# Optimization experiments

Measured on AMD Instinct MI355X. Metric: run time of the kernel, lower is better.

## Reference

```python
import jax, jax.numpy as jnp
import numpy as np

D = 32          # embedding_size
B = 16384       # batch_size
P = 16          # neighbor_sample_size (paths per item per hop)
NE = 100000     # n_entity
NU = 100000     # n_user
NR = 32         # n_relation
N_ITER = 2


def setup_inputs() -> dict:
    key = jax.random.key(0)
    ks = jax.random.split(key, 20)
    s = 0.1
    nrm = lambda k, sh: jax.random.normal(k, sh, dtype=jnp.float32) * s
    inp = {
        "user_table": nrm(ks[0], (NU, D)),
        "ent_table": nrm(ks[1], (NE, D)),
        "rel_table": nrm(ks[2], (NR, D)),
        # PyTorch LSTM params, gate order (i, f, g, o)
        "w_ih0": nrm(ks[3], (4 * D, 2 * D)),
        "w_hh0": nrm(ks[4], (4 * D, D)),
        "b_ih0": nrm(ks[5], (4 * D,)),
        "b_hh0": nrm(ks[6], (4 * D,)),
        "w_ih1": nrm(ks[7], (4 * D, 2 * D)),
        "w_hh1": nrm(ks[8], (4 * D, D)),
        "b_ih1": nrm(ks[9], (4 * D,)),
        "b_hh1": nrm(ks[10], (4 * D,)),
        "agg_w": nrm(ks[11], (D, D)),
        "agg_b": nrm(ks[12], (D,)),
        "users": jax.random.randint(ks[13], (B,), 0, NU),
        "items": jax.random.randint(ks[14], (B,), 0, NE),
        "ratings": jax.random.randint(ks[15], (B,), 0, 2),
        # hop h path table: [n_entity, P, 2*(h+1)+1]; values < 32 valid for both tables
        "lp0": jax.random.randint(ks[16], (NE, P, 3), 0, 32),
        "lp1": jax.random.randint(ks[17], (NE, P, 5), 0, 32),
    }
    return inp


def _lstm_last(seq, w_ih, w_hh, b_ih, b_hh):
    # seq: [N, T, 2D] -> final hidden state [N, D], PyTorch gate order i,f,g,o
    N = seq.shape[0]
    H = w_hh.shape[1]
    bias = b_ih + b_hh

    def step(carry, x):
        h, c = carry
        g = x @ w_ih.T + h @ w_hh.T + bias
        i, f, gg, o = jnp.split(g, 4, axis=-1)
        c = jax.nn.sigmoid(f) * c + jax.nn.sigmoid(i) * jnp.tanh(gg)
        h = jax.nn.sigmoid(o) * jnp.tanh(c)
        return (h, c), None

    h0 = jnp.zeros((N, H), seq.dtype)
    (h, _), _ = jax.lax.scan(step, (h0, h0), jnp.swapaxes(seq, 0, 1))
    return h


def _forward(user_table, ent_table, rel_table, lstm_params, agg_w, agg_b,
             users, items, ratings, lps):
    u = user_table[users]                # [B, D]
    items_emb = ent_table[items]         # [B, D]
    for hop in range(N_ITER):
        lp = lps[hop]
        w_ih, w_hh, b_ih, b_hh = lstm_params[hop]
        il = lp[items]                   # [B, P, 2*(hop+1)+1]
        seed_e = ent_table[il[:, :, 0]]  # [B, P, D]
        u_b = jnp.broadcast_to(u[:, None, :], seed_e.shape)
        first = jnp.concatenate([u_b, seed_e], -1)[:, :, None, :]   # [B,P,1,2D]
        rel_e = rel_table[il[:, :, 1::2]]                            # [B,P,hop+1,D]
        tail_e = ent_table[il[:, :, 2::2]]                           # [B,P,hop+1,D]
        rest = jnp.concatenate([rel_e, tail_e], -1)                  # [B,P,hop+1,2D]
        seq = jnp.concatenate([first, rest], 2).reshape(B * P, hop + 2, 2 * D)
        h = _lstm_last(seq, w_ih, w_hh, b_ih, b_hh)                  # [B*P, D]
        final = h.reshape(B, P, D).sum(axis=1)                       # hidden_out sum
        items_emb = (items_emb + final) @ agg_w.T + agg_b            # 'sum' aggregator
    scores = jnp.sum(u * items_emb, axis=-1)                         # [B]
    r = ratings.astype(scores.dtype)
    # stable BCE on sigmoid(scores)
    loss = -jnp.mean(r * jax.nn.log_sigmoid(scores) + (1.0 - r) * jax.nn.log_sigmoid(-scores))
    return loss, jax.nn.sigmoid(scores)


def reference(user_table, ent_table, rel_table,
              w_ih0, w_hh0, b_ih0, b_hh0,
              w_ih1, w_hh1, b_ih1, b_hh1,
              agg_w, agg_b,
              users, items, ratings, lp0, lp1):
    lstm_params = [(w_ih0, w_hh0, b_ih0, b_hh0), (w_ih1, w_hh1, b_ih1, b_hh1)]
    loss, scores_normalized = _forward(user_table, ent_table, rel_table,
                                       lstm_params, agg_w, agg_b,
                                       users, items, ratings, (lp0, lp1))
    return (loss, scores_normalized, items)
```

## Files before the change

### kernel.cpp

```cpp
#include <hip/hip_runtime.h>
#include <math.h>

#define D  32
#define BN 16384
#define PP 16

typedef __bf16 bf16x8 __attribute__((ext_vector_type(8)));
typedef float  floatx4 __attribute__((ext_vector_type(4)));

#define IMG_BYTES   29184
#define WIH_OFF     0
#define WHH_OFF     18432
#define BIAS_OFF    28672
#define X_OFF       29184
#define H_OFF       38400
#define LDS_BYTES   43520

__device__ __forceinline__ float sigf(float x) {
    float e = __builtin_amdgcn_exp2f(-x * 1.44269504088896341f);
    return __builtin_amdgcn_rcpf(1.0f + e);
}
__device__ __forceinline__ float tanh_fast(float x) {
    float e = __builtin_amdgcn_exp2f(x * 2.88539008177792681f);
    return 1.0f - 2.0f * __builtin_amdgcn_rcpf(e + 1.0f);
}
__device__ __forceinline__ float logsigf(float x) {
    float ax = fabsf(x);
    float l = log1pf(__expf(-ax));
    return (x >= 0.0f) ? -l : x - l;
}

__device__ __forceinline__ void stage16(const float* __restrict__ src, char* dst) {
    const float4* s = (const float4*)src;
    float4 a = s[0], b = s[1], c = s[2], d = s[3];
    bf16x8 lo = { (__bf16)a.x, (__bf16)a.y, (__bf16)a.z, (__bf16)a.w,
                  (__bf16)b.x, (__bf16)b.y, (__bf16)b.z, (__bf16)b.w };
    bf16x8 hi = { (__bf16)c.x, (__bf16)c.y, (__bf16)c.z, (__bf16)c.w,
                  (__bf16)d.x, (__bf16)d.y, (__bf16)d.z, (__bf16)d.w };
    *(bf16x8*)dst        = lo;
    *(bf16x8*)(dst + 16) = hi;
}

__global__ __launch_bounds__(256)
void prep_weights(const float* __restrict__ w_ih, const float* __restrict__ w_hh,
                  const float* __restrict__ b_ih, const float* __restrict__ b_hh,
                  float* __restrict__ img_f)
{
    char* base = (char*)img_f;
    const int t0 = blockIdx.x * 256 + threadIdx.x;
    for (int idx = t0; idx < 8192; idx += 2048) {
        int n = idx >> 6, k = idx & 63;
        ((__bf16*)(base + WIH_OFF))[n * 72 + k] = (__bf16)w_ih[idx];
    }
    for (int idx = t0; idx < 4096; idx += 2048) {
        int n = idx >> 5, k = idx & 31;
        ((__bf16*)(base + WHH_OFF))[n * 40 + k] = (__bf16)w_hh[idx];
    }
    if (t0 < 128)
        ((float*)(base + BIAS_OFF))[t0] = b_ih[t0] + b_hh[t0];
}

template<int L, int T>
__global__ __launch_bounds__(256, 2)
void hop_mfma(const float* __restrict__ user_table,
              const float* __restrict__ ent_table,
              const float* __restrict__ rel_table,
              const float* __restrict__ img,
              const int*   __restrict__ users,
              const int*   __restrict__ items,
              const int*   __restrict__ lp,
              float* __restrict__ final_out)
{
    __shared__ __align__(16) char lds[LDS_BYTES];

    const int tid  = threadIdx.x;
    const int lane = tid & 63;
    const int wave = tid >> 6;

    {
        const float4* g = (const float4*)img;
        float4* l = (float4*)lds;
        #pragma unroll
        for (int i = 0; i < 8; ++i) {
            int idx = i * 256 + tid;
            if (idx < IMG_BYTES / 16) l[idx] = g[idx];
        }
    }
    __syncthreads();

    char* Wih  = lds + WIH_OFF;
    char* Whh  = lds + WHH_OFF;
    const float* bias = (const float*)(lds + BIAS_OFF);
    char* Xl   = lds + X_OFF;
    char* Hl   = lds + H_OFF;

    const int srow  = tid >> 2;
    const int squad = tid & 3;
    const int spair = blockIdx.x * 64 + srow;
    const int sb    = spair >> 4;
    const int sp    = spair & 15;
    const int sitem = items[sb];
    const int suser = users[sb];
    const int* __restrict__ sil = lp + ((size_t)sitem * PP + sp) * L;
    char* sdst = Xl + srow * 144 + squad * 32;

    const int wrow = wave * 16;
    const int am   = wrow + (lane & 15);
    const int ak   = (lane >> 4) * 8;
    const int bnl  = lane & 15;

    float cst[8]  = {0,0,0,0,0,0,0,0};
    float hout[8];
    floatx4 acc[8];
    #pragma unroll
    for (int nt = 0; nt < 8; ++nt) {
        float bv = bias[nt * 16 + bnl];
        floatx4 v = { bv, bv, bv, bv };
        acc[nt] = v;
    }

    #pragma unroll
    for (int t = 0; t < T; ++t) {
        {
            const float* src;
            if (t == 0) {
                src = (squad < 2) ? user_table + (size_t)suser * D + squad * 16
                                  : ent_table + (size_t)sil[0] * D + (squad - 2) * 16;
            } else {
                src = (squad < 2) ? rel_table + (size_t)sil[2 * t - 1] * D + squad * 16
                                  : ent_table + (size_t)sil[2 * t]     * D + (squad - 2) * 16;
            }
            stage16(src, sdst);
        }

        bf16x8 ax0 = *(const bf16x8*)(Xl + am * 144 + ak * 2);
        bf16x8 ax1 = *(const bf16x8*)(Xl + am * 144 + 64 + ak * 2);
        bf16x8 ah  = {};
        if (t > 0) ah = *(const bf16x8*)(Hl + am * 80 + ak * 2);

        #pragma unroll
        for (int nt = 0; nt < 8; ++nt) {
            const int bn = nt * 16 + bnl;
            bf16x8 b0 = *(const bf16x8*)(Wih + bn * 144 + ak * 2);
            bf16x8 b1 = *(const bf16x8*)(Wih + bn * 144 + 64 + ak * 2);
            floatx4 a = acc[nt];
            a = __builtin_amdgcn_mfma_f32_16x16x32_bf16(ax0, b0, a, 0, 0, 0);
            a = __builtin_amdgcn_mfma_f32_16x16x32_bf16(ax1, b1, a, 0, 0, 0);
            if (t > 0) {
                bf16x8 bh = *(const bf16x8*)(Whh + bn * 80 + ak * 2);
                a = __builtin_amdgcn_mfma_f32_16x16x32_bf16(ah, bh, a, 0, 0, 0);
            }
            acc[nt] = a;
        }

        #pragma unroll
        for (int ng = 0; ng < 2; ++ng) {
            floatx4 gi = acc[ng], gf = acc[ng + 2], gg = acc[ng + 4], go = acc[ng + 6];
            #pragma unroll
            for (int r = 0; r < 4; ++r) {
                float c = cst[ng * 4 + r];
                c = sigf(gf[r]) * c + sigf(gi[r]) * tanh_fast(gg[r]);
                cst[ng * 4 + r] = c;
                float h = sigf(go[r]) * tanh_fast(c);
                hout[ng * 4 + r] = h;
                if (t < T - 1) {
                    int pr = wrow + (lane >> 4) * 4 + r;
                    int un = ng * 16 + bnl;
                    *(__bf16*)(Hl + pr * 80 + un * 2) = (__bf16)h;
                }
            }
        }

        if (t < T - 1) {
            #pragma unroll
            for (int nt = 0; nt < 8; ++nt) {
                float bv = bias[nt * 16 + bnl];
                floatx4 v = { bv, bv, bv, bv };
                acc[nt] = v;
            }
        }
    }

    const int fb = blockIdx.x * 4 + wave;
    #pragma unroll
    for (int ng = 0; ng < 2; ++ng) {
        float v = hout[ng * 4 + 0] + hout[ng * 4 + 1] + hout[ng * 4 + 2] + hout[ng * 4 + 3];
        v += __shfl_xor(v, 16);
        v += __shfl_xor(v, 32);
        if (lane < 16)
            final_out[(size_t)fb * D + ng * 16 + lane] = v;
    }
}

__global__ __launch_bounds__(256)
void agg_kernel(const float* __restrict__ src_emb,
                const float* __restrict__ ent_table,
                const int*   __restrict__ items,
                const float* __restrict__ final_in,
                const float* __restrict__ agg_w,
                const float* __restrict__ agg_b,
                float* __restrict__ out_emb)
{
    const int t = blockIdx.x * 256 + threadIdx.x;
    const int b = t >> 5;
    const int j = t & 31;
    const float* __restrict__ src =
        src_emb ? (src_emb + (size_t)b * D) : (ent_table + (size_t)items[b] * D);
    const float* __restrict__ fin = final_in + (size_t)b * D;
    const float* __restrict__ w   = agg_w + (size_t)j * D;
    float acc = agg_b[j];
    #pragma unroll
    for (int k = 0; k < D; ++k) acc = fmaf(src[k] + fin[k], w[k], acc);
    out_emb[t] = acc;
}

__global__ __launch_bounds__(256)
void score_kernel(const float* __restrict__ user_table,
                  const float* __restrict__ emb,
                  const int*   __restrict__ users,
                  const int*   __restrict__ items,
                  const int*   __restrict__ ratings,
                  float* __restrict__ out,
                  float* __restrict__ partials)
{
    __shared__ float red[4];
    const int t = threadIdx.x;
    const int b = blockIdx.x * 256 + t;
    const float* __restrict__ u = user_table + (size_t)users[b] * D;
    const float* __restrict__ e = emb + (size_t)b * D;
    float s = 0.0f;
    #pragma unroll
    for (int k = 0; k < D; ++k) s = fmaf(u[k], e[k], s);
    out[1 + b]      = sigf(s);
    out[1 + BN + b] = (float)items[b];
    float r = (float)ratings[b];
    float term = r * logsigf(s) + (1.0f - r) * logsigf(-s);
    #pragma unroll
    for (int m = 1; m < 64; m <<= 1) term += __shfl_xor(term, m);
    if ((t & 63) == 0) red[t >> 6] = term;
    __syncthreads();
    if (t == 0) partials[blockIdx.x] = red[0] + red[1] + red[2] + red[3];
}

__global__ void loss_kernel(const float* __restrict__ partials, float* __restrict__ out)
{
    const int t = threadIdx.x;
    float v = partials[t];
    #pragma unroll
    for (int m = 1; m < 64; m <<= 1) v += __shfl_xor(v, m);
    if (t == 0) out[0] = -v / (float)BN;
}

extern "C" void kernel_launch(void* const* d_in, const int* in_sizes, int n_in,
                              void* d_out, int out_size, void* d_ws, size_t ws_size,
                              hipStream_t stream)
{
    const float* user_table = (const float*)d_in[0];
    const float* ent_table  = (const float*)d_in[1];
    const float* rel_table  = (const float*)d_in[2];
    const float* w_ih0 = (const float*)d_in[3];
    const float* w_hh0 = (const float*)d_in[4];
    const float* b_ih0 = (const float*)d_in[5];
    const float* b_hh0 = (const float*)d_in[6];
    const float* w_ih1 = (const float*)d_in[7];
    const float* w_hh1 = (const float*)d_in[8];
    const float* b_ih1 = (const float*)d_in[9];
    const float* b_hh1 = (const float*)d_in[10];
    const float* agg_w = (const float*)d_in[11];
    const float* agg_b = (const float*)d_in[12];
    const int* users   = (const int*)d_in[13];
    const int* items   = (const int*)d_in[14];
    const int* ratings = (const int*)d_in[15];
    const int* lp0     = (const int*)d_in[16];
    const int* lp1     = (const int*)d_in[17];
    float* out = (float*)d_out;

    float* ws        = (float*)d_ws;
    float* final_buf = ws;
    float* emb0      = ws + (size_t)BN * D;
    float* emb1      = ws + 2 * (size_t)BN * D;
    float* partials  = ws + 3 * (size_t)BN * D;
    float* img0      = ws + 3 * (size_t)BN * D + 64;
    float* img1      = img0 + IMG_BYTES / 4;

    prep_weights<<<8, 256, 0, stream>>>(w_ih0, w_hh0, b_ih0, b_hh0, img0);
    prep_weights<<<8, 256, 0, stream>>>(w_ih1, w_hh1, b_ih1, b_hh1, img1);

    const int hop_blocks = (BN * PP) / 64;
    hop_mfma<3, 2><<<hop_blocks, 256, 0, stream>>>(
        user_table, ent_table, rel_table, img0, users, items, lp0, final_buf);
    agg_kernel<<<(BN * D) / 256, 256, 0, stream>>>(
        nullptr, ent_table, items, final_buf, agg_w, agg_b, emb0);
    hop_mfma<5, 3><<<hop_blocks, 256, 0, stream>>>(
        user_table, ent_table, rel_table, img1, users, items, lp1, final_buf);
    agg_kernel<<<(BN * D) / 256, 256, 0, stream>>>(
        emb0, ent_table, items, final_buf, agg_w, agg_b, emb1);
    score_kernel<<<BN / 256, 256, 0, stream>>>(
        user_table, emb1, users, items, ratings, out, partials);
    loss_kernel<<<1, 64, 0, stream>>>(partials, out);
}
```

Measured before the change: 249.3 us.

## Fuse both LSTM hops into one launch and fuse aggregation with scoring

Runs both hop LSTMs in a single kernel, with interleaved blocks selecting the hop, since the hop-1 LSTM does not depend on hop-0 results. Input fragments are loaded directly from global memory into MFMA registers instead of being staged through LDS. Gate activations are rewritten to share reciprocals. Both aggregation steps and scoring are fused into one kernel, and the weight prep launches are merged. This cuts launch count and intermediate global traffic, at the cost of some uncoalesced gathers and mixed workloads within one grid.

```diff
diff --git a/kernel.cpp b/kernel.cpp
--- a/kernel.cpp
+++ b/kernel.cpp
@@ -8,21 +8,19 @@
 typedef __bf16 bf16x8 __attribute__((ext_vector_type(8)));
 typedef float  floatx4 __attribute__((ext_vector_type(4)));
 
-#define IMG_BYTES   29184
 #define WIH_OFF     0
 #define WHH_OFF     18432
 #define BIAS_OFF    28672
-#define X_OFF       29184
-#define H_OFF       38400
-#define LDS_BYTES   43520
+#define IMG_BYTES   29184
+#define H_OFF       IMG_BYTES
+#define LDS_BYTES   (IMG_BYTES + 5120)
+
+#define K1 1.44269504088896341f
+#define K2 2.88539008177792681f
 
 __device__ __forceinline__ float sigf(float x) {
-    float e = __builtin_amdgcn_exp2f(-x * 1.44269504088896341f);
+    float e = __builtin_amdgcn_exp2f(-x * K1);
     return __builtin_amdgcn_rcpf(1.0f + e);
-}
-__device__ __forceinline__ float tanh_fast(float x) {
-    float e = __builtin_amdgcn_exp2f(x * 2.88539008177792681f);
-    return 1.0f - 2.0f * __builtin_amdgcn_rcpf(e + 1.0f);
 }
 __device__ __forceinline__ float logsigf(float x) {
     float ax = fabsf(x);
@@ -30,24 +28,31 @@
     return (x >= 0.0f) ? -l : x - l;
 }
 
-__device__ __forceinline__ void stage16(const float* __restrict__ src, char* dst) {
-    const float4* s = (const float4*)src;
-    float4 a = s[0], b = s[1], c = s[2], d = s[3];
-    bf16x8 lo = { (__bf16)a.x, (__bf16)a.y, (__bf16)a.z, (__bf16)a.w,
-                  (__bf16)b.x, (__bf16)b.y, (__bf16)b.z, (__bf16)b.w };
-    bf16x8 hi = { (__bf16)c.x, (__bf16)c.y, (__bf16)c.z, (__bf16)c.w,
-                  (__bf16)d.x, (__bf16)d.y, (__bf16)d.z, (__bf16)d.w };
-    *(bf16x8*)dst        = lo;
-    *(bf16x8*)(dst + 16) = hi;
+__device__ __forceinline__ bf16x8 cvt8(float4 lo, float4 hi) {
+    bf16x8 r = { (__bf16)lo.x, (__bf16)lo.y, (__bf16)lo.z, (__bf16)lo.w,
+                 (__bf16)hi.x, (__bf16)hi.y, (__bf16)hi.z, (__bf16)hi.w };
+    return r;
+}
+__device__ __forceinline__ bf16x8 load_frag(const float* __restrict__ tab,
+                                            int row, int ak) {
+    const float4* p = (const float4*)(tab + (size_t)row * D) + (ak >> 2);
+    return cvt8(p[0], p[1]);
 }
 
 __global__ __launch_bounds__(256)
-void prep_weights(const float* __restrict__ w_ih, const float* __restrict__ w_hh,
-                  const float* __restrict__ b_ih, const float* __restrict__ b_hh,
-                  float* __restrict__ img_f)
-{
-    char* base = (char*)img_f;
-    const int t0 = blockIdx.x * 256 + threadIdx.x;
+void prep_weights(const float* __restrict__ w_ih0, const float* __restrict__ w_hh0,
+                  const float* __restrict__ b_ih0, const float* __restrict__ b_hh0,
+                  const float* __restrict__ w_ih1, const float* __restrict__ w_hh1,
+                  const float* __restrict__ b_ih1, const float* __restrict__ b_hh1,
+                  float* __restrict__ img0, float* __restrict__ img1)
+{
+    const bool second = blockIdx.x >= 8;
+    const float* w_ih = second ? w_ih1 : w_ih0;
+    const float* w_hh = second ? w_hh1 : w_hh0;
+    const float* b_ih = second ? b_ih1 : b_ih0;
+    const float* b_hh = second ? b_hh1 : b_hh0;
+    char* base = (char*)(second ? img1 : img0);
+    const int t0 = (blockIdx.x & 7) * 256 + threadIdx.x;
     for (int idx = t0; idx < 8192; idx += 2048) {
         int n = idx >> 6, k = idx & 63;
         ((__bf16*)(base + WIH_OFF))[n * 72 + k] = (__bf16)w_ih[idx];
@@ -60,195 +65,217 @@
         ((float*)(base + BIAS_OFF))[t0] = b_ih[t0] + b_hh[t0];
 }
 
-template<int L, int T>
+template<bool FIRST, bool LAST>
+__device__ __forceinline__ void lstm_step(
+    const char* __restrict__ Wih, const char* __restrict__ Whh, char* __restrict__ Hl,
+    bf16x8 ax0, bf16x8 ax1, const float* __restrict__ biasv,
+    float* __restrict__ cst, float* __restrict__ hout,
+    int bnl, int ak, int am, int wrow, int lane)
+{
+    bf16x8 ah = {};
+    if (!FIRST) ah = *(const bf16x8*)(Hl + am * 80 + ak * 2);
+
+    floatx4 acc[8];
+    #pragma unroll
+    for (int nt = 0; nt < 8; ++nt) {
+        floatx4 v = { biasv[nt], biasv[nt], biasv[nt], biasv[nt] };
+        acc[nt] = v;
+    }
+    #pragma unroll
+    for (int nt = 0; nt < 8; ++nt) {
+        const int bn = nt * 16 + bnl;
+        bf16x8 b0 = *(const bf16x8*)(Wih + bn * 144 + ak * 2);
+        bf16x8 b1 = *(const bf16x8*)(Wih + bn * 144 + 64 + ak * 2);
+        floatx4 a = acc[nt];
+        a = __builtin_amdgcn_mfma_f32_16x16x32_bf16(ax0, b0, a, 0, 0, 0);
+        a = __builtin_amdgcn_mfma_f32_16x16x32_bf16(ax1, b1, a, 0, 0, 0);
+        if (!FIRST) {
+            bf16x8 bh = *(const bf16x8*)(Whh + bn * 80 + ak * 2);
+            a = __builtin_amdgcn_mfma_f32_16x16x32_bf16(ah, bh, a, 0, 0, 0);
+        }
+        acc[nt] = a;
+    }
+
+    #pragma unroll
+    for (int ng = 0; ng < 2; ++ng) {
+        floatx4 gi = acc[ng], gf = acc[ng + 2], gg = acc[ng + 4], go = acc[ng + 6];
+        #pragma unroll
+        for (int r = 0; r < 4; ++r) {
+            float Ai = 1.0f + __builtin_amdgcn_exp2f(-gi[r] * K1);
+            float Af = 1.0f + __builtin_amdgcn_exp2f(-gf[r] * K1);
+            float G2 = __builtin_amdgcn_exp2f(gg[r] * K2);
+            float Gp = G2 + 1.0f, Gm = G2 - 1.0f;
+            float cold = FIRST ? 0.0f : cst[ng * 4 + r];
+            float num = cold * Ai * Gp + Gm * Af;
+            float c = num * __builtin_amdgcn_rcpf(Af * Ai * Gp);
+            cst[ng * 4 + r] = c;
+            float Ao = 1.0f + __builtin_amdgcn_exp2f(-go[r] * K1);
+            float C2 = __builtin_amdgcn_exp2f(c * K2);
+            float h = (C2 - 1.0f) * __builtin_amdgcn_rcpf(Ao * (C2 + 1.0f));
+            hout[ng * 4 + r] = h;
+            if (!LAST) {
+                int pr = wrow + (lane >> 4) * 4 + r;
+                *(__bf16*)(Hl + pr * 80 + (ng * 16 + bnl) * 2) = (__bf16)h;
+            }
+        }
+    }
+}
+
 __global__ __launch_bounds__(256, 2)
 void hop_mfma(const float* __restrict__ user_table,
               const float* __restrict__ ent_table,
               const float* __restrict__ rel_table,
-              const float* __restrict__ img,
+              const float* __restrict__ img0,
+              const float* __restrict__ img1,
               const int*   __restrict__ users,
               const int*   __restrict__ items,
-              const int*   __restrict__ lp,
-              float* __restrict__ final_out)
+              const int*   __restrict__ lp0,
+              const int*   __restrict__ lp1,
+              float* __restrict__ F0,
+              float* __restrict__ F1)
 {
     __shared__ __align__(16) char lds[LDS_BYTES];
 
+    const bool second = blockIdx.x & 1;
+    const int  idx    = blockIdx.x >> 1;
     const int tid  = threadIdx.x;
     const int lane = tid & 63;
     const int wave = tid >> 6;
 
     {
-        const float4* g = (const float4*)img;
+        const float4* g = (const float4*)(second ? img1 : img0);
         float4* l = (float4*)lds;
         #pragma unroll
         for (int i = 0; i < 8; ++i) {
-            int idx = i * 256 + tid;
-            if (idx < IMG_BYTES / 16) l[idx] = g[idx];
+            int k = i * 256 + tid;
+            if (k < IMG_BYTES / 16) l[k] = g[k];
         }
     }
-    __syncthreads();
-
-    char* Wih  = lds + WIH_OFF;
-    char* Whh  = lds + WHH_OFF;
-    const float* bias = (const float*)(lds + BIAS_OFF);
-    char* Xl   = lds + X_OFF;
-    char* Hl   = lds + H_OFF;
-
-    const int srow  = tid >> 2;
-    const int squad = tid & 3;
-    const int spair = blockIdx.x * 64 + srow;
-    const int sb    = spair >> 4;
-    const int sp    = spair & 15;
-    const int sitem = items[sb];
-    const int suser = users[sb];
-    const int* __restrict__ sil = lp + ((size_t)sitem * PP + sp) * L;
-    char* sdst = Xl + srow * 144 + squad * 32;
-
+
+    const char* Wih = lds + WIH_OFF;
+    const char* Whh = lds + WHH_OFF;
+    char* Hl = lds + H_OFF;
+
+    const int bnl  = lane & 15;
+    const int ak   = (lane >> 4) * 8;
     const int wrow = wave * 16;
-    const int am   = wrow + (lane & 15);
-    const int ak   = (lane >> 4) * 8;
-    const int bnl  = lane & 15;
-
-    float cst[8]  = {0,0,0,0,0,0,0,0};
-    float hout[8];
-    floatx4 acc[8];
-    #pragma unroll
-    for (int nt = 0; nt < 8; ++nt) {
-        float bv = bias[nt * 16 + bnl];
-        floatx4 v = { bv, bv, bv, bv };
-        acc[nt] = v;
-    }
-
-    #pragma unroll
-    for (int t = 0; t < T; ++t) {
-        {
-            const float* src;
-            if (t == 0) {
-                src = (squad < 2) ? user_table + (size_t)suser * D + squad * 16
-                                  : ent_table + (size_t)sil[0] * D + (squad - 2) * 16;
-            } else {
-                src = (squad < 2) ? rel_table + (size_t)sil[2 * t - 1] * D + squad * 16
-                                  : ent_table + (size_t)sil[2 * t]     * D + (squad - 2) * 16;
-            }
-            stage16(src, sdst);
+    const int am   = wrow + bnl;
+
+    const int fb   = idx * 4 + wave;
+    const int item = items[fb];
+    const int user = users[fb];
+    const int* __restrict__ il = (second ? lp1 : lp0)
+        + ((size_t)item * PP + bnl) * (second ? 5 : 3);
+
+    bf16x8 xa0, xb0, xa1, xb1, xa2 = {}, xb2 = {};
+    {
+        const int i0 = il[0];
+        xa0 = load_frag(user_table, user, ak);
+        xb0 = load_frag(ent_table, i0, ak);
+        const int i1 = il[1], i2 = il[2];
+        xa1 = load_frag(rel_table, i1, ak);
+        xb1 = load_frag(ent_table, i2, ak);
+        if (second) {
+            const int i3 = il[3], i4 = il[4];
+            xa2 = load_frag(rel_table, i3, ak);
+            xb2 = load_frag(ent_table, i4, ak);
         }
-
-        bf16x8 ax0 = *(const bf16x8*)(Xl + am * 144 + ak * 2);
-        bf16x8 ax1 = *(const bf16x8*)(Xl + am * 144 + 64 + ak * 2);
-        bf16x8 ah  = {};
-        if (t > 0) ah = *(const bf16x8*)(Hl + am * 80 + ak * 2);
-
+    }
+
+    __syncthreads();
+
+    float biasv[8];
+    {
+        const float* bias = (const float*)(lds + BIAS_OFF);
         #pragma unroll
-        for (int nt = 0; nt < 8; ++nt) {
-            const int bn = nt * 16 + bnl;
-            bf16x8 b0 = *(const bf16x8*)(Wih + bn * 144 + ak * 2);
-            bf16x8 b1 = *(const bf16x8*)(Wih + bn * 144 + 64 + ak * 2);
-            floatx4 a = acc[nt];
-            a = __builtin_amdgcn_mfma_f32_16x16x32_bf16(ax0, b0, a, 0, 0, 0);
-            a = __builtin_amdgcn_mfma_f32_16x16x32_bf16(ax1, b1, a, 0, 0, 0);
-            if (t > 0) {
-                bf16x8 bh = *(const bf16x8*)(Whh + bn * 80 + ak * 2);
-                a = __builtin_amdgcn_mfma_f32_16x16x32_bf16(ah, bh, a, 0, 0, 0);
-            }
-            acc[nt] = a;
-        }
-
-        #pragma unroll
-        for (int ng = 0; ng < 2; ++ng) {
-            floatx4 gi = acc[ng], gf = acc[ng + 2], gg = acc[ng + 4], go = acc[ng + 6];
-            #pragma unroll
-            for (int r = 0; r < 4; ++r) {
-                float c = cst[ng * 4 + r];
-                c = sigf(gf[r]) * c + sigf(gi[r]) * tanh_fast(gg[r]);
-                cst[ng * 4 + r] = c;
-                float h = sigf(go[r]) * tanh_fast(c);
-                hout[ng * 4 + r] = h;
-                if (t < T - 1) {
-                    int pr = wrow + (lane >> 4) * 4 + r;
-                    int un = ng * 16 + bnl;
-                    *(__bf16*)(Hl + pr * 80 + un * 2) = (__bf16)h;
-                }
-            }
-        }
-
-        if (t < T - 1) {
-            #pragma unroll
-            for (int nt = 0; nt < 8; ++nt) {
-                float bv = bias[nt * 16 + bnl];
-                floatx4 v = { bv, bv, bv, bv };
-                acc[nt] = v;
-            }
-        }
-    }
-
-    const int fb = blockIdx.x * 4 + wave;
+        for (int nt = 0; nt < 8; ++nt) biasv[nt] = bias[nt * 16 + bnl];
+    }
+
+    float cst[8], hout[8];
+    lstm_step<true, false>(Wih, Whh, Hl, xa0, xb0, biasv, cst, hout, bnl, ak, am, wrow, lane);
+    if (!second) {
+        lstm_step<false, true>(Wih, Whh, Hl, xa1, xb1, biasv, cst, hout, bnl, ak, am, wrow, lane);
+    } else {
+        lstm_step<false, false>(Wih, Whh, Hl, xa1, xb1, biasv, cst, hout, bnl, ak, am, wrow, lane);
+        lstm_step<false, true >(Wih, Whh, Hl, xa2, xb2, biasv, cst, hout, bnl, ak, am, wrow, lane);
+    }
+
+    float* Fout = second ? F1 : F0;
     #pragma unroll
     for (int ng = 0; ng < 2; ++ng) {
         float v = hout[ng * 4 + 0] + hout[ng * 4 + 1] + hout[ng * 4 + 2] + hout[ng * 4 + 3];
         v += __shfl_xor(v, 16);
         v += __shfl_xor(v, 32);
         if (lane < 16)
-            final_out[(size_t)fb * D + ng * 16 + lane] = v;
+            Fout[(size_t)fb * D + ng * 16 + lane] = v;
     }
 }
 
 __global__ __launch_bounds__(256)
-void agg_kernel(const float* __restrict__ src_emb,
-                const float* __restrict__ ent_table,
-                const int*   __restrict__ items,
-                const float* __restrict__ final_in,
-                const float* __restrict__ agg_w,
-                const float* __restrict__ agg_b,
-                float* __restrict__ out_emb)
-{
-    const int t = blockIdx.x * 256 + threadIdx.x;
-    const int b = t >> 5;
-    const int j = t & 31;
-    const float* __restrict__ src =
-        src_emb ? (src_emb + (size_t)b * D) : (ent_table + (size_t)items[b] * D);
-    const float* __restrict__ fin = final_in + (size_t)b * D;
-    const float* __restrict__ w   = agg_w + (size_t)j * D;
-    float acc = agg_b[j];
-    #pragma unroll
-    for (int k = 0; k < D; ++k) acc = fmaf(src[k] + fin[k], w[k], acc);
-    out_emb[t] = acc;
+void chain_score(const float* __restrict__ user_table,
+                 const float* __restrict__ ent_table,
+                 const float* __restrict__ agg_w,
+                 const float* __restrict__ agg_b,
+                 const int*   __restrict__ users,
+                 const int*   __restrict__ items,
+                 const int*   __restrict__ ratings,
+                 const float* __restrict__ F0,
+                 const float* __restrict__ F1,
+                 float* __restrict__ out,
+                 float* __restrict__ partials)
+{
+    __shared__ float s[8][33];
+    __shared__ float red[8];
+    const int tid = threadIdx.x;
+    const int bb  = tid >> 5;
+    const int j   = tid & 31;
+    const int b   = blockIdx.x * 8 + bb;
+    const int it  = items[b];
+
+    s[bb][j] = ent_table[(size_t)it * D + j] + F0[(size_t)b * D + j];
+    __syncthreads();
+    const float* __restrict__ w = agg_w + (size_t)j * D;
+    float e0 = agg_b[j];
+    #pragma unroll
+    for (int k = 0; k < D; ++k) e0 = fmaf(s[bb][k], w[k], e0);
+    __syncthreads();
+    s[bb][j] = e0 + F1[(size_t)b * D + j];
+    __syncthreads();
+    float e1 = agg_b[j];
+    #pragma unroll
+    for (int k = 0; k < D; ++k) e1 = fmaf(s[bb][k], w[k], e1);
+
+    float prod = user_table[(size_t)users[b] * D + j] * e1;
+    #pragma unroll
+    for (int m = 1; m < 32; m <<= 1) prod += __shfl_xor(prod, m);
+    if (j == 0) {
+        out[1 + b]      = sigf(prod);
+        out[1 + BN + b] = (float)it;
+        float r = (float)ratings[b];
+        red[bb] = r * logsigf(prod) + (1.0f - r) * logsigf(-prod);
+    }
+    __syncthreads();
+    if (tid == 0) {
+        float t = 0.0f;
+        #pragma unroll
+        for (int q = 0; q < 8; ++q) t += red[q];
+        partials[blockIdx.x] = t;
+    }
 }
 
 __global__ __launch_bounds__(256)
-void score_kernel(const float* __restrict__ user_table,
-                  const float* __restrict__ emb,
-                  const int*   __restrict__ users,
-                  const int*   __restrict__ items,
-                  const int*   __restrict__ ratings,
-                  float* __restrict__ out,
-                  float* __restrict__ partials)
+void loss_kernel(const float* __restrict__ partials, float* __restrict__ out)
 {
     __shared__ float red[4];
     const int t = threadIdx.x;
-    const int b = blockIdx.x * 256 + t;
-    const float* __restrict__ u = user_table + (size_t)users[b] * D;
-    const float* __restrict__ e = emb + (size_t)b * D;
-    float s = 0.0f;
-    #pragma unroll
-    for (int k = 0; k < D; ++k) s = fmaf(u[k], e[k], s);
-    out[1 + b]      = sigf(s);
-    out[1 + BN + b] = (float)items[b];
-    float r = (float)ratings[b];
-    float term = r * logsigf(s) + (1.0f - r) * logsigf(-s);
-    #pragma unroll
-    for (int m = 1; m < 64; m <<= 1) term += __shfl_xor(term, m);
-    if ((t & 63) == 0) red[t >> 6] = term;
-    __syncthreads();
-    if (t == 0) partials[blockIdx.x] = red[0] + red[1] + red[2] + red[3];
-}
-
-__global__ void loss_kernel(const float* __restrict__ partials, float* __restrict__ out)
-{
-    const int t = threadIdx.x;
-    float v = partials[t];
+    float v = 0.0f;
+    #pragma unroll
+    for (int q = 0; q < 8; ++q) v += partials[q * 256 + t];
     #pragma unroll
     for (int m = 1; m < 64; m <<= 1) v += __shfl_xor(v, m);
-    if (t == 0) out[0] = -v / (float)BN;
+    if ((t & 63) == 0) red[t >> 6] = v;
+    __syncthreads();
+    if (t == 0) out[0] = -(red[0] + red[1] + red[2] + red[3]) / (float)BN;
 }
 
 extern "C" void kernel_launch(void* const* d_in, const int* in_sizes, int n_in,
@@ -275,27 +302,20 @@
     const int* lp1     = (const int*)d_in[17];
     float* out = (float*)d_out;
 
-    float* ws        = (float*)d_ws;
-    float* final_buf = ws;
-    float* emb0      = ws + (size_t)BN * D;
-    float* emb1      = ws + 2 * (size_t)BN * D;
-    float* partials  = ws + 3 * (size_t)BN * D;
-    float* img0      = ws + 3 * (size_t)BN * D + 64;
-    float* img1      = img0 + IMG_BYTES / 4;
-
-    prep_weights<<<8, 256, 0, stream>>>(w_ih0, w_hh0, b_ih0, b_hh0, img0);
-    prep_weights<<<8, 256, 0, stream>>>(w_ih1, w_hh1, b_ih1, b_hh1, img1);
-
-    const int hop_blocks = (BN * PP) / 64;
-    hop_mfma<3, 2><<<hop_blocks, 256, 0, stream>>>(
-        user_table, ent_table, rel_table, img0, users, items, lp0, final_buf);
-    agg_kernel<<<(BN * D) / 256, 256, 0, stream>>>(
-        nullptr, ent_table, items, final_buf, agg_w, agg_b, emb0);
-    hop_mfma<5, 3><<<hop_blocks, 256, 0, stream>>>(
-        user_table, ent_table, rel_table, img1, users, items, lp1, final_buf);
-    agg_kernel<<<(BN * D) / 256, 256, 0, stream>>>(
-        emb0, ent_table, items, final_buf, agg_w, agg_b, emb1);
-    score_kernel<<<BN / 256, 256, 0, stream>>>(
-        user_table, emb1, users, items, ratings, out, partials);
-    loss_kernel<<<1, 64, 0, stream>>>(partials, out);
-}
+    float* ws       = (float*)d_ws;
+    float* F0       = ws;
+    float* F1       = ws + (size_t)BN * D;
+    float* partials = ws + 2 * (size_t)BN * D;
+    float* img0     = ws + 2 * (size_t)BN * D + 2048;
+    float* img1     = img0 + IMG_BYTES / 4;
+
+    prep_weights<<<16, 256, 0, stream>>>(w_ih0, w_hh0, b_ih0, b_hh0,
+                                         w_ih1, w_hh1, b_ih1, b_hh1, img0, img1);
+    hop_mfma<<<8192, 256, 0, stream>>>(
+        user_table, ent_table, rel_table, img0, img1,
+        users, items, lp0, lp1, F0, F1);
+    chain_score<<<BN / 8, 256, 0, stream>>>(
+        user_table, ent_table, agg_w, agg_b, users, items, ratings,
+        F0, F1, out, partials);
+    loss_kernel<<<1, 256, 0, stream>>>(partials, out);
+}
```

Result: no change. 254.3 us (+2.0%).
